# Kernel tuning notes

Measured on AMD Instinct MI355X. Metric: run time of the kernel, lower is better.

Reference implementation:

```python
import jax, jax.numpy as jnp
import numpy as np
import math

B, L, Cs, Cz, Ch, H, Pq, Pv, NB = 1, 768, 384, 128, 16, 12, 4, 8, 30
INF = 100000.0
EPS = 1e-8
HC = H * Ch
CONCAT = H * (Cz + Ch + Pv * 4)


def setup_inputs() -> dict:
    key = jax.random.key(0)
    ks = jax.random.split(key, 24)
    s = jax.random.normal(ks[0], (B, L, Cs), jnp.float32)
    z = jax.random.normal(ks[1], (B, L, NB, Cz), jnp.float32)
    # random orthonormal frames (QR of gaussian) -> valid rigid rotations
    m = jax.random.normal(ks[2], (B, L, 3, 3), jnp.float32)
    rot, _ = jnp.linalg.qr(m)
    trans = jax.random.normal(ks[3], (B, L, 3), jnp.float32) * 10.0
    mask = jnp.ones((B, L), jnp.float32)
    # unique neighbor indices per residue (scatter with duplicate targets is ill-defined)
    E_idx = jnp.argsort(jax.random.uniform(ks[4], (B, L, L)), axis=-1)[..., :NB].astype(jnp.int64)
    sc = 0.02
    W_q = jax.random.normal(ks[5], (Cs, HC), jnp.float32) * sc
    b_q = jnp.zeros((HC,), jnp.float32)
    W_kv = jax.random.normal(ks[6], (Cs, 2 * HC), jnp.float32) * sc
    b_kv = jnp.zeros((2 * HC,), jnp.float32)
    W_qp = jax.random.normal(ks[7], (Cs, H * Pq * 3), jnp.float32) * sc
    b_qp = jnp.zeros((H * Pq * 3,), jnp.float32)
    W_kvp = jax.random.normal(ks[8], (Cs, H * (Pq + Pv) * 3), jnp.float32) * sc
    b_kvp = jnp.zeros((H * (Pq + Pv) * 3,), jnp.float32)
    W_b = jax.random.normal(ks[9], (Cz, H), jnp.float32) * sc
    b_b = jnp.zeros((H,), jnp.float32)
    head_weights = jax.random.normal(ks[10], (H,), jnp.float32) * 0.5 + 0.5
    W_out = jax.random.normal(ks[11], (CONCAT, Cs), jnp.float32) * sc
    b_out = jnp.zeros((Cs,), jnp.float32)
    return dict(s=s, z=z, rot=rot, trans=trans, mask=mask, E_idx=E_idx,
                W_q=W_q, b_q=b_q, W_kv=W_kv, b_kv=b_kv, W_qp=W_qp, b_qp=b_qp,
                W_kvp=W_kvp, b_kvp=b_kvp, W_b=W_b, b_b=b_b,
                head_weights=head_weights, W_out=W_out, b_out=b_out)


def _ipa(s, z, rot, trans, mask, E_idx, W_q, b_q, W_kv, b_kv, W_qp, b_qp,
         W_kvp, b_kvp, W_b, b_b, head_weights, W_out, b_out):
    # scatter neighbor pair features into dense [B, L, L, Cz] (module's z_padding.scatter)
    b_ix = jnp.arange(B)[:, None, None]
    i_ix = jnp.arange(L)[None, :, None]
    z_dense = jnp.zeros((B, L, L, Cz), z.dtype).at[b_ix, i_ix, E_idx].set(z)

    q = (s @ W_q + b_q).reshape(B, L, H, Ch)
    kv = (s @ W_kv + b_kv).reshape(B, L, H, 2 * Ch)
    k, v = kv[..., :Ch], kv[..., Ch:]

    def to_points(flat, P):
        # split into 3 coordinate chunks, stack on last dim -> [B, L, H*P, 3]
        p = jnp.stack(jnp.split(flat, 3, axis=-1), axis=-1)
        # rigid apply: R @ p + t
        p = jnp.einsum('blij,blpj->blpi', rot, p) + trans[:, :, None, :]
        return p.reshape(B, L, H, P, 3)

    q_pts = to_points(s @ W_qp + b_qp, Pq)              # [B,L,H,Pq,3]
    kv_pts = to_points(s @ W_kvp + b_kvp, Pq + Pv)
    k_pts, v_pts = kv_pts[..., :Pq, :], kv_pts[..., Pq:, :]

    bias = z_dense @ W_b + b_b                          # [B,L,L,H]
    a = jnp.einsum('bihc,bjhc->bhij', q, k) * math.sqrt(1.0 / (3 * Ch))
    a = a + math.sqrt(1.0 / 3) * bias.transpose(0, 3, 1, 2)

    # squared point distances [B,L,L,H,Pq]
    diff = q_pts[:, :, None] - k_pts[:, None]           # [B,L,L,H,Pq,3]
    pt_att = jnp.sum(diff * diff, axis=-1)
    hw = jax.nn.softplus(head_weights) * math.sqrt(1.0 / (3 * (Pq * 9.0 / 2)))
    pt_att = jnp.sum(pt_att * hw[None, None, None, :, None], axis=-1) * (-0.5)  # [B,L,L,H]

    sq_mask = INF * (mask[:, :, None] * mask[:, None, :] - 1.0)
    a = a + pt_att.transpose(0, 3, 1, 2) + sq_mask[:, None]
    a = jax.nn.softmax(a, axis=-1)                      # [B,H,L,L]

    o = jnp.einsum('bhij,bjhc->bihc', a, v).reshape(B, L, HC)
    o_pt = jnp.einsum('bhij,bjhpc->bihpc', a, v_pts)    # [B,L,H,Pv,3]
    # rigid invert_apply: R^T (x - t)
    o_pt = jnp.einsum('blji,blhpj->blhpi', rot, o_pt - trans[:, :, None, None, :])
    o_pt_norm = jnp.sqrt(jnp.sum(o_pt ** 2, axis=-1) + EPS).reshape(B, L, H * Pv)
    o_pt = o_pt.reshape(B, L, H * Pv, 3)
    o_pair = jnp.einsum('bhij,bijc->bihc', a, z_dense).reshape(B, L, H * Cz)

    cat = jnp.concatenate(
        [o, o_pt[..., 0], o_pt[..., 1], o_pt[..., 2], o_pt_norm, o_pair], axis=-1)
    return cat @ W_out + b_out


def reference(s, z, rot, trans, mask, E_idx, W_q, b_q, W_kv, b_kv, W_qp, b_qp,
              W_kvp, b_kvp, W_b, b_b, head_weights, W_out, b_out):
    return _ipa(s, z, rot, trans, mask, E_idx, W_q, b_q, W_kv, b_kv, W_qp, b_qp,
                W_kvp, b_kvp, W_b, b_b, head_weights, W_out, b_out)
```

## Files before the change

### kernel.cpp

```cpp
#include <hip/hip_runtime.h>
#include <hip/hip_bf16.h>
#include <math.h>

#define L_    768
#define Cs_   384
#define Cz_   128
#define H_    12
#define NB_   30
#define CONCAT_ 2112
#define PROJN 1152

#define SCALE_QK  0.14433756729740643f
#define SQRT3INV  0.5773502691896258f
#define WC_       0.13608276348795434f
#define INF_      100000.0f

typedef short bf16x8 __attribute__((ext_vector_type(8)));
typedef float f32x4 __attribute__((ext_vector_type(4)));

__device__ __forceinline__ short f2b(float f) {
  __hip_bfloat16 b = __float2bfloat16(f);
  return *reinterpret_cast<short*>(&b);
}
__device__ __forceinline__ float b2f(short s) {
  __hip_bfloat16 b;
  *reinterpret_cast<short*>(&b) = s;
  return __bfloat162float(b);
}

__global__ void pack_kernel(const float* __restrict__ Wq, const float* __restrict__ bq,
                            const float* __restrict__ Wkv, const float* __restrict__ bkv,
                            const float* __restrict__ Wqp, const float* __restrict__ bqp,
                            const float* __restrict__ Wkvp, const float* __restrict__ bkvp,
                            short* __restrict__ WallT, float* __restrict__ ball) {
  int e = blockIdx.x * 256 + threadIdx.x;
  if (e < Cs_ * PROJN) {
    int col = e / 384, kk = e % 384;
    float v;
    if (col < 192)      v = Wq[kk*192 + col];
    else if (col < 576) v = Wkv[kk*384 + (col-192)];
    else if (col < 720) v = Wqp[kk*144 + (col-576)];
    else                v = Wkvp[kk*432 + (col-720)];
    WallT[e] = f2b(v);
  } else if (e < Cs_ * PROJN + PROJN) {
    int col = e - Cs_ * PROJN;
    float v;
    if (col < 192)      v = bq[col];
    else if (col < 576) v = bkv[col-192];
    else if (col < 720) v = bqp[col-576];
    else                v = bkvp[col-720];
    ball[col] = v;
  }
}

__global__ void cvt_s(const float* __restrict__ s, short* __restrict__ sb) {
  int e = blockIdx.x * 256 + threadIdx.x;
  if (e < L_ * Cs_) sb[e] = f2b(s[e]);
}

__global__ __launch_bounds__(64) void proj_mfma(const short* __restrict__ A,
                                                const short* __restrict__ Bt,
                                                const float* __restrict__ bias,
                                                float* __restrict__ C) {
  const int l = threadIdx.x, r = l & 15, kg = l >> 4;
  const int m0 = blockIdx.x * 16, n0 = blockIdx.y * 16;
  const short* ap = A  + (size_t)(m0 + r) * 384 + kg * 8;
  const short* bp = Bt + (size_t)(n0 + r) * 384 + kg * 8;
  f32x4 acc = {0.f, 0.f, 0.f, 0.f};
  #pragma unroll
  for (int k = 0; k < 12; ++k) {
    bf16x8 af = *(const bf16x8*)(ap + k * 32);
    bf16x8 bf = *(const bf16x8*)(bp + k * 32);
    acc = __builtin_amdgcn_mfma_f32_16x16x32_bf16(af, bf, acc, 0, 0, 0);
  }
  const float bv = bias[n0 + r];
  #pragma unroll
  for (int j = 0; j < 4; ++j)
    C[(size_t)(m0 + kg * 4 + j) * PROJN + n0 + r] = acc[j] + bv;
}

__global__ __launch_bounds__(256) void prep_kernel(const float* __restrict__ proj,
                                                   const float* __restrict__ rot,
                                                   const float* __restrict__ trans,
                                                   const float* __restrict__ maskp,
                                                   const float* __restrict__ head_w,
                                                   short* __restrict__ Amat,
                                                   short* __restrict__ Bmat,
                                                   short* __restrict__ VmatT,
                                                   float* __restrict__ colbias) {
  const int h = blockIdx.x / 3;
  const int i = (blockIdx.x % 3) * 256 + threadIdx.x;
  const float* p = proj + (size_t)i * PROJN;
  const float* R = rot + i * 9;
  const float* T = trans + i * 3;
  const float c2 = log1pf(expf(head_w[h])) * WC_;
  short* arow = Amat + ((size_t)h * L_ + i) * 64;
  short* brow = Bmat + ((size_t)h * L_ + i) * 64;
  #pragma unroll
  for (int c = 0; c < 16; ++c) {
    arow[c] = f2b(p[h * 16 + c] * SCALE_QK);
    brow[c] = f2b(p[192 + h * 32 + c]);
    VmatT[((size_t)h * 64 + c) * L_ + i] = f2b(p[192 + h * 32 + 16 + c]);
  }
  #pragma unroll
  for (int pt = 0; pt < 4; ++pt) {
    int idx = h * 4 + pt;
    float lx = p[576 + idx], ly = p[576 + 48 + idx], lz = p[576 + 96 + idx];
    float g[3];
    g[0] = R[0]*lx + R[1]*ly + R[2]*lz + T[0];
    g[1] = R[3]*lx + R[4]*ly + R[5]*lz + T[1];
    g[2] = R[6]*lx + R[7]*ly + R[8]*lz + T[2];
    #pragma unroll
    for (int d = 0; d < 3; ++d) {
      float x = c2 * g[d];
      short xh = f2b(x);
      short xl = f2b(x - b2f(xh));
      arow[16 + pt*3 + d] = xh; arow[28 + pt*3 + d] = xh;
      arow[40 + pt*3 + d] = xl; arow[52 + pt*3 + d] = xl;
    }
  }
  float s2 = 0.f;
  #pragma unroll
  for (int pt = 0; pt < 4; ++pt) {
    int idx = h * 12 + pt;
    float lx = p[720 + idx], ly = p[720 + 144 + idx], lz = p[720 + 288 + idx];
    float g[3];
    g[0] = R[0]*lx + R[1]*ly + R[2]*lz + T[0];
    g[1] = R[3]*lx + R[4]*ly + R[5]*lz + T[1];
    g[2] = R[6]*lx + R[7]*ly + R[8]*lz + T[2];
    #pragma unroll
    for (int d = 0; d < 3; ++d) {
      s2 += g[d] * g[d];
      short kh = f2b(g[d]);
      short kl = f2b(g[d] - b2f(kh));
      brow[16 + pt*3 + d] = kh; brow[28 + pt*3 + d] = kl;
      brow[40 + pt*3 + d] = kh; brow[52 + pt*3 + d] = kl;
    }
  }
  colbias[h * L_ + i] = -0.5f * c2 * s2 + INF_ * (maskp[i] - 1.0f);
  #pragma unroll
  for (int pt = 4; pt < 12; ++pt) {
    int idx = h * 12 + pt;
    float lx = p[720 + idx], ly = p[720 + 144 + idx], lz = p[720 + 288 + idx];
    float g[3];
    g[0] = R[0]*lx + R[1]*ly + R[2]*lz + T[0];
    g[1] = R[3]*lx + R[4]*ly + R[5]*lz + T[1];
    g[2] = R[6]*lx + R[7]*ly + R[8]*lz + T[2];
    #pragma unroll
    for (int d = 0; d < 3; ++d) {
      int pc = (pt - 4) * 3 + d;
      short vh = f2b(g[d]);
      short vl = f2b(g[d] - b2f(vh));
      VmatT[((size_t)h * 64 + 16 + pc) * L_ + i] = vh;
      VmatT[((size_t)h * 64 + 40 + pc) * L_ + i] = vl;
    }
  }
}

__global__ __launch_bounds__(256) void bias_edge_kernel(const float* __restrict__ z,
                                                        const float* __restrict__ Wb,
                                                        float* __restrict__ bias_e) {
  int i = blockIdx.x;
  __shared__ float zs[NB_ * 129];
  __shared__ float wbs[Cz_ * H_];
  int t = threadIdx.x;
  for (int e = t; e < NB_ * Cz_; e += 256) { int k = e >> 7, c = e & 127; zs[k * 129 + c] = z[(size_t)i * NB_ * Cz_ + e]; }
  for (int e = t; e < Cz_ * H_; e += 256) wbs[e] = Wb[e];
  __syncthreads();
  for (int o = t; o < NB_ * H_; o += 256) {
    int k = o / H_, hh = o % H_;
    float a0 = 0.f, a1 = 0.f, a2 = 0.f, a3 = 0.f;
    #pragma unroll
    for (int c = 0; c < 128; c += 4) {
      a0 += zs[k*129 + c    ] * wbs[(c    ) * H_ + hh];
      a1 += zs[k*129 + c + 1] * wbs[(c + 1) * H_ + hh];
      a2 += zs[k*129 + c + 2] * wbs[(c + 2) * H_ + hh];
      a3 += zs[k*129 + c + 3] * wbs[(c + 3) * H_ + hh];
    }
    bias_e[(size_t)i * NB_ * H_ + o] = SQRT3INV * ((a0 + a1) + (a2 + a3));
  }
}

#define SLS 772
__global__ __launch_bounds__(256) void attn_mfma(
    const short* __restrict__ Amat,
    const short* __restrict__ Bmat,
    const short* __restrict__ VmatT,
    const float* __restrict__ colbias,
    const float* __restrict__ bias_e,
    const int*   __restrict__ E_idx,
    const float* __restrict__ rot,
    const float* __restrict__ trans,
    const float* __restrict__ z,
    short* __restrict__ catb)
{
  const int h = blockIdx.y;
  const int i0 = blockIdx.x * 16;
  const int t = threadIdx.x;
  const int lane = t & 63, wave = t >> 6;
  const int fr = lane & 15, kg = lane >> 4;

  __shared__ __align__(16) float Sl[16][SLS];
  __shared__ float ptb[16][48];
  __shared__ float ews[16][NB_];
  __shared__ int   eidx[16][NB_];
  __shared__ float denom[16];

  const short* Ab = Amat + ((size_t)h * L_ + i0 + fr) * 64 + kg * 8;
  bf16x8 a0 = *(const bf16x8*)(Ab);
  bf16x8 a1 = *(const bf16x8*)(Ab + 32);

  for (int e = t; e < 16 * NB_; e += 256)
    eidx[e / NB_][e % NB_] = E_idx[(i0 + e / NB_) * NB_ + e % NB_];

  #pragma unroll 3
  for (int tt = 0; tt < 12; ++tt) {
    const int j0 = wave * 192 + tt * 16;
    const short* Bb = Bmat + ((size_t)h * L_ + j0 + fr) * 64 + kg * 8;
    f32x4 acc = {0.f, 0.f, 0.f, 0.f};
    acc = __builtin_amdgcn_mfma_f32_16x16x32_bf16(a0, *(const bf16x8*)(Bb), acc, 0, 0, 0);
    acc = __builtin_amdgcn_mfma_f32_16x16x32_bf16(a1, *(const bf16x8*)(Bb + 32), acc, 0, 0, 0);
    const float cb = colbias[h * L_ + j0 + fr];
    #pragma unroll
    for (int j = 0; j < 4; ++j)
      Sl[kg * 4 + j][j0 + fr] = acc[j] + cb;
  }
  __syncthreads();

  for (int e = t; e < 16 * NB_; e += 256) {
    int r = e / NB_, k = e % NB_;
    Sl[r][eidx[r][k]] += bias_e[(size_t)((i0 + r) * NB_ + k) * H_ + h];
  }
  __syncthreads();

  {
    const int r = t >> 4, sub = t & 15;
    float mx = -1e30f;
    #pragma unroll
    for (int n = 0; n < 48; ++n) mx = fmaxf(mx, Sl[r][sub + n * 16]);
    #pragma unroll
    for (int d = 8; d; d >>= 1) mx = fmaxf(mx, __shfl_xor(mx, d, 16));
    float sum = 0.f;
    #pragma unroll
    for (int n = 0; n < 48; ++n) {
      float p = __expf(Sl[r][sub + n * 16] - mx);
      Sl[r][sub + n * 16] = p;
      sum += p;
    }
    #pragma unroll
    for (int d = 8; d; d >>= 1) sum += __shfl_xor(sum, d, 16);
    if (sub == 0) denom[r] = sum;
  }
  __syncthreads();

  for (int e = t; e < 16 * NB_; e += 256) {
    int r = e / NB_, k = e % NB_;
    ews[r][k] = Sl[r][eidx[r][k]];
  }

  f32x4 oacc = {0.f, 0.f, 0.f, 0.f};
  const short* Vb = VmatT + ((size_t)h * 64 + wave * 16 + fr) * L_ + kg * 8;
  #pragma unroll 4
  for (int ks = 0; ks < 24; ++ks) {
    const float* sp = &Sl[fr][ks * 32 + kg * 8];
    float4 u = *(const float4*)sp;
    float4 v = *(const float4*)(sp + 4);
    bf16x8 pa;
    pa[0] = f2b(u.x); pa[1] = f2b(u.y); pa[2] = f2b(u.z); pa[3] = f2b(u.w);
    pa[4] = f2b(v.x); pa[5] = f2b(v.y); pa[6] = f2b(v.z); pa[7] = f2b(v.w);
    bf16x8 vb = *(const bf16x8*)(Vb + ks * 32);
    oacc = __builtin_amdgcn_mfma_f32_16x16x32_bf16(pa, vb, oacc, 0, 0, 0);
  }
  if (wave == 0) {
    #pragma unroll
    for (int j = 0; j < 4; ++j) {
      int r = kg * 4 + j;
      catb[(size_t)(i0 + r) * CONCAT_ + h * 16 + fr] = f2b(oacc[j] / denom[r]);
    }
  } else {
    int ch = wave * 16 + fr;
    int dest = (ch < 40) ? (ch - 16) : (24 + ch - 40);
    #pragma unroll
    for (int j = 0; j < 4; ++j)
      ptb[kg * 4 + j][dest] = oacc[j];
  }
  __syncthreads();

  if (t < 128) {
    int r = t >> 3, pt = t & 7;
    int ii = i0 + r;
    float di = 1.0f / denom[r];
    const float* T = trans + ii * 3;
    float gx = (ptb[r][pt * 3 + 0] + ptb[r][24 + pt * 3 + 0]) * di - T[0];
    float gy = (ptb[r][pt * 3 + 1] + ptb[r][24 + pt * 3 + 1]) * di - T[1];
    float gz = (ptb[r][pt * 3 + 2] + ptb[r][24 + pt * 3 + 2]) * di - T[2];
    const float* R = rot + ii * 9;
    float lx = R[0] * gx + R[3] * gy + R[6] * gz;
    float ly = R[1] * gx + R[4] * gy + R[7] * gz;
    float lz = R[2] * gx + R[5] * gy + R[8] * gz;
    float nrm = sqrtf(lx * lx + ly * ly + lz * lz + 1e-8f);
    short* crow = catb + (size_t)ii * CONCAT_;
    crow[192 + h * 8 + pt] = f2b(lx);
    crow[288 + h * 8 + pt] = f2b(ly);
    crow[384 + h * 8 + pt] = f2b(lz);
    crow[480 + h * 8 + pt] = f2b(nrm);
  }

  {
    const int r = t >> 4, sub = t & 15;
    const int ii = i0 + r;
    const float di = 1.0f / denom[r];
    float accs[8];
    #pragma unroll
    for (int n = 0; n < 8; ++n) accs[n] = 0.f;
    #pragma unroll 5
    for (int k = 0; k < NB_; ++k) {
      float w = ews[r][k];
      const float* zp = z + ((size_t)ii * NB_ + k) * Cz_ + sub;
      #pragma unroll
      for (int n = 0; n < 8; ++n) accs[n] += w * zp[n * 16];
    }
    short* crow = catb + (size_t)ii * CONCAT_ + 576 + h * Cz_;
    #pragma unroll
    for (int n = 0; n < 8; ++n) crow[sub + n * 16] = f2b(accs[n] * di);
  }
}

__global__ __launch_bounds__(256) void cvt_wout(const float* __restrict__ W, short* __restrict__ Wt) {
  __shared__ float tile[32][33];
  const int k0 = blockIdx.x * 32, n0 = blockIdx.y * 32;
  const int tn = threadIdx.x & 31, tk = threadIdx.x >> 5;
  #pragma unroll
  for (int kk = tk; kk < 32; kk += 8)
    tile[kk][tn] = W[(size_t)(k0 + kk) * Cs_ + n0 + tn];
  __syncthreads();
  #pragma unroll
  for (int rr = tk; rr < 32; rr += 8)
    Wt[(size_t)(n0 + rr) * CONCAT_ + k0 + tn] = f2b(tile[tn][rr]);
}

__global__ __launch_bounds__(64) void gemm_out_mfma(const short* __restrict__ A,
                                                    const short* __restrict__ Bt,
                                                    const float* __restrict__ bias,
                                                    float* __restrict__ C) {
  const int l = threadIdx.x;
  const int r = l & 15, kg = l >> 4;
  const int m0 = blockIdx.x * 16, n0 = blockIdx.y * 16;
  const short* ap = A  + (size_t)(m0 + r) * CONCAT_ + kg * 8;
  const short* bp = Bt + (size_t)(n0 + r) * CONCAT_ + kg * 8;
  f32x4 acc = {0.f, 0.f, 0.f, 0.f};
  #pragma unroll 6
  for (int k = 0; k < 66; ++k) {
    bf16x8 af = *(const bf16x8*)(ap + k * 32);
    bf16x8 bf = *(const bf16x8*)(bp + k * 32);
    acc = __builtin_amdgcn_mfma_f32_16x16x32_bf16(af, bf, acc, 0, 0, 0);
  }
  const float bv = bias[n0 + r];
  #pragma unroll
  for (int j = 0; j < 4; ++j)
    C[(size_t)(m0 + kg * 4 + j) * Cs_ + n0 + r] = acc[j] + bv;
}

extern "C" void kernel_launch(void* const* d_in, const int* in_sizes, int n_in,
                              void* d_out, int out_size, void* d_ws, size_t ws_size,
                              hipStream_t stream) {
  const float* s      = (const float*)d_in[0];
  const float* z      = (const float*)d_in[1];
  const float* rot    = (const float*)d_in[2];
  const float* trans  = (const float*)d_in[3];
  const float* mask   = (const float*)d_in[4];
  const int*   E      = (const int*)  d_in[5];
  const float* W_q    = (const float*)d_in[6];
  const float* b_q    = (const float*)d_in[7];
  const float* W_kv   = (const float*)d_in[8];
  const float* b_kv   = (const float*)d_in[9];
  const float* W_qp   = (const float*)d_in[10];
  const float* b_qp   = (const float*)d_in[11];
  const float* W_kvp  = (const float*)d_in[12];
  const float* b_kvp  = (const float*)d_in[13];
  const float* W_b    = (const float*)d_in[14];
  const float* b_b    = (const float*)d_in[15];  (void)b_b;
  const float* head_w = (const float*)d_in[16];
  const float* W_out  = (const float*)d_in[17];
  const float* b_out  = (const float*)d_in[18];

  float* ws = (float*)d_ws;
  short* WallT   = (short*)(ws + 0);
  float* ball    = ws + 221184;
  short* sb      = (short*)(ws + 222336);
  float* proj    = ws + 369792;
  short* catb    = (short*)(ws + 0);
  short* WoutT   = (short*)(ws + 811008);
  short* Amat    = (short*)(ws + 1254528);
  short* Bmat    = (short*)(ws + 1549440);
  short* VmatT   = (short*)(ws + 1844352);
  float* colbias = ws + 2139264;
  float* bias_e  = ws + 2148480;

  pack_kernel<<<(Cs_ * PROJN + PROJN + 255) / 256, 256, 0, stream>>>(
      W_q, b_q, W_kv, b_kv, W_qp, b_qp, W_kvp, b_kvp, WallT, ball);

  cvt_s<<<(L_ * Cs_ + 255) / 256, 256, 0, stream>>>(s, sb);

  proj_mfma<<<dim3(L_ / 16, PROJN / 16), 64, 0, stream>>>(sb, WallT, ball, proj);

  prep_kernel<<<36, 256, 0, stream>>>(proj, rot, trans, mask, head_w, Amat, Bmat, VmatT, colbias);

  cvt_wout<<<dim3(CONCAT_ / 32, Cs_ / 32), 256, 0, stream>>>(W_out, WoutT);

  bias_edge_kernel<<<L_, 256, 0, stream>>>(z, W_b, bias_e);

  attn_mfma<<<dim3(L_ / 16, H_), 256, 0, stream>>>(
      Amat, Bmat, VmatT, colbias, bias_e, E, rot, trans, z, catb);

  gemm_out_mfma<<<dim3(L_ / 16, Cs_ / 16), 64, 0, stream>>>(catb, WoutT, b_out, (float*)d_out);
}
```

Measured before the change: 192.6 us.

## Split-K output GEMM, MFMA edge bias, pre-packed bf16 P, fused s conversion

The output GEMM now splits its 66 k-steps across four waves per block and reduces the partials in shared memory, so each block has more waves to hide latency. The edge-bias projection becomes a bf16 MFMA over z rows instead of a scalar shared-memory loop. The attention kernel converts the softmax probabilities to packed bf16 in place once, so the PV loop no longer converts them on every k-step. The s conversion is folded into the weight-pack kernel to remove one launch. The edge bias is now computed in bf16 rather than fp32, which lowers its precision.

```diff
diff --git a/kernel.cpp b/kernel.cpp
--- a/kernel.cpp
+++ b/kernel.cpp
@@ -32,7 +32,9 @@
                             const float* __restrict__ Wkv, const float* __restrict__ bkv,
                             const float* __restrict__ Wqp, const float* __restrict__ bqp,
                             const float* __restrict__ Wkvp, const float* __restrict__ bkvp,
-                            short* __restrict__ WallT, float* __restrict__ ball) {
+                            const float* __restrict__ s,
+                            short* __restrict__ WallT, float* __restrict__ ball,
+                            short* __restrict__ sb) {
   int e = blockIdx.x * 256 + threadIdx.x;
   if (e < Cs_ * PROJN) {
     int col = e / 384, kk = e % 384;
@@ -50,12 +52,10 @@
     else if (col < 720) v = bqp[col-576];
     else                v = bkvp[col-720];
     ball[col] = v;
-  }
-}
-
-__global__ void cvt_s(const float* __restrict__ s, short* __restrict__ sb) {
-  int e = blockIdx.x * 256 + threadIdx.x;
-  if (e < L_ * Cs_) sb[e] = f2b(s[e]);
+  } else if (e < Cs_ * PROJN + PROJN + L_ * Cs_) {
+    int x = e - (Cs_ * PROJN + PROJN);
+    sb[x] = f2b(s[x]);
+  }
 }
 
 __global__ __launch_bounds__(64) void proj_mfma(const short* __restrict__ A,
@@ -157,27 +157,31 @@
   }
 }
 
-__global__ __launch_bounds__(256) void bias_edge_kernel(const float* __restrict__ z,
-                                                        const float* __restrict__ Wb,
-                                                        float* __restrict__ bias_e) {
-  int i = blockIdx.x;
-  __shared__ float zs[NB_ * 129];
-  __shared__ float wbs[Cz_ * H_];
-  int t = threadIdx.x;
-  for (int e = t; e < NB_ * Cz_; e += 256) { int k = e >> 7, c = e & 127; zs[k * 129 + c] = z[(size_t)i * NB_ * Cz_ + e]; }
-  for (int e = t; e < Cz_ * H_; e += 256) wbs[e] = Wb[e];
-  __syncthreads();
-  for (int o = t; o < NB_ * H_; o += 256) {
-    int k = o / H_, hh = o % H_;
-    float a0 = 0.f, a1 = 0.f, a2 = 0.f, a3 = 0.f;
-    #pragma unroll
-    for (int c = 0; c < 128; c += 4) {
-      a0 += zs[k*129 + c    ] * wbs[(c    ) * H_ + hh];
-      a1 += zs[k*129 + c + 1] * wbs[(c + 1) * H_ + hh];
-      a2 += zs[k*129 + c + 2] * wbs[(c + 2) * H_ + hh];
-      a3 += zs[k*129 + c + 3] * wbs[(c + 3) * H_ + hh];
-    }
-    bias_e[(size_t)i * NB_ * H_ + o] = SQRT3INV * ((a0 + a1) + (a2 + a3));
+__global__ __launch_bounds__(64) void bias_mfma(const float* __restrict__ z,
+                                                const float* __restrict__ Wb,
+                                                float* __restrict__ bias_e) {
+  const int l = threadIdx.x, r = l & 15, kg = l >> 4;
+  const int m0 = blockIdx.x * 16;
+  f32x4 acc = {0.f, 0.f, 0.f, 0.f};
+  const float* zr = z + (size_t)(m0 + r) * Cz_ + kg * 8;
+  #pragma unroll
+  for (int kc = 0; kc < 4; ++kc) {
+    float4 a0 = *(const float4*)(zr + kc * 32);
+    float4 a1 = *(const float4*)(zr + kc * 32 + 4);
+    bf16x8 af, bf;
+    af[0]=f2b(a0.x); af[1]=f2b(a0.y); af[2]=f2b(a0.z); af[3]=f2b(a0.w);
+    af[4]=f2b(a1.x); af[5]=f2b(a1.y); af[6]=f2b(a1.z); af[7]=f2b(a1.w);
+    #pragma unroll
+    for (int j = 0; j < 8; ++j) {
+      int k = kc * 32 + kg * 8 + j;
+      bf[j] = (r < H_) ? f2b(Wb[k * H_ + r]) : (short)0;
+    }
+    acc = __builtin_amdgcn_mfma_f32_16x16x32_bf16(af, bf, acc, 0, 0, 0);
+  }
+  if (r < H_) {
+    #pragma unroll
+    for (int j = 0; j < 4; ++j)
+      bias_e[(size_t)(m0 + kg * 4 + j) * H_ + r] = SQRT3INV * acc[j];
   }
 }
 
@@ -257,17 +261,32 @@
     int r = e / NB_, k = e % NB_;
     ews[r][k] = Sl[r][eidx[r][k]];
   }
+  {
+    const int cr = t & 15;
+    const int cc = (t >> 4) * 48;
+    float v[48];
+    #pragma unroll
+    for (int n = 0; n < 12; ++n) {
+      float4 u = *(const float4*)&Sl[cr][cc + n * 4];
+      v[n*4+0] = u.x; v[n*4+1] = u.y; v[n*4+2] = u.z; v[n*4+3] = u.w;
+    }
+    __syncthreads();
+    unsigned* dst = (unsigned*)&Sl[cr][0];
+    #pragma unroll
+    for (int n = 0; n < 24; ++n) {
+      unsigned lo = (unsigned short)f2b(v[2*n]);
+      unsigned hi = (unsigned short)f2b(v[2*n+1]);
+      dst[cc/2 + n] = lo | (hi << 16);
+    }
+  }
+  __syncthreads();
 
   f32x4 oacc = {0.f, 0.f, 0.f, 0.f};
   const short* Vb = VmatT + ((size_t)h * 64 + wave * 16 + fr) * L_ + kg * 8;
+  const short* PbRow = (const short*)&Sl[fr][0];
   #pragma unroll 4
   for (int ks = 0; ks < 24; ++ks) {
-    const float* sp = &Sl[fr][ks * 32 + kg * 8];
-    float4 u = *(const float4*)sp;
-    float4 v = *(const float4*)(sp + 4);
-    bf16x8 pa;
-    pa[0] = f2b(u.x); pa[1] = f2b(u.y); pa[2] = f2b(u.z); pa[3] = f2b(u.w);
-    pa[4] = f2b(v.x); pa[5] = f2b(v.y); pa[6] = f2b(v.z); pa[7] = f2b(v.w);
+    bf16x8 pa = *(const bf16x8*)(PbRow + ks * 32 + kg * 8);
     bf16x8 vb = *(const bf16x8*)(Vb + ks * 32);
     oacc = __builtin_amdgcn_mfma_f32_16x16x32_bf16(pa, vb, oacc, 0, 0, 0);
   }
@@ -339,26 +358,33 @@
     Wt[(size_t)(n0 + rr) * CONCAT_ + k0 + tn] = f2b(tile[tn][rr]);
 }
 
-__global__ __launch_bounds__(64) void gemm_out_mfma(const short* __restrict__ A,
-                                                    const short* __restrict__ Bt,
-                                                    const float* __restrict__ bias,
-                                                    float* __restrict__ C) {
-  const int l = threadIdx.x;
+__global__ __launch_bounds__(256) void gemm_out_mfma(const short* __restrict__ A,
+                                                     const short* __restrict__ Bt,
+                                                     const float* __restrict__ bias,
+                                                     float* __restrict__ C) {
+  const int t = threadIdx.x;
+  const int w = t >> 6, l = t & 63;
   const int r = l & 15, kg = l >> 4;
   const int m0 = blockIdx.x * 16, n0 = blockIdx.y * 16;
-  const short* ap = A  + (size_t)(m0 + r) * CONCAT_ + kg * 8;
-  const short* bp = Bt + (size_t)(n0 + r) * CONCAT_ + kg * 8;
+  __shared__ float part[4][16][17];
+  const int kcnt = (w < 2) ? 17 : 16;
+  const int koff = (w < 2) ? w * 17 : 34 + (w - 2) * 16;
+  const short* ap = A  + (size_t)(m0 + r) * CONCAT_ + koff * 32 + kg * 8;
+  const short* bp = Bt + (size_t)(n0 + r) * CONCAT_ + koff * 32 + kg * 8;
   f32x4 acc = {0.f, 0.f, 0.f, 0.f};
-  #pragma unroll 6
-  for (int k = 0; k < 66; ++k) {
+  #pragma unroll 4
+  for (int k = 0; k < kcnt; ++k) {
     bf16x8 af = *(const bf16x8*)(ap + k * 32);
     bf16x8 bf = *(const bf16x8*)(bp + k * 32);
     acc = __builtin_amdgcn_mfma_f32_16x16x32_bf16(af, bf, acc, 0, 0, 0);
   }
-  const float bv = bias[n0 + r];
-  #pragma unroll
-  for (int j = 0; j < 4; ++j)
-    C[(size_t)(m0 + kg * 4 + j) * Cs_ + n0 + r] = acc[j] + bv;
+  #pragma unroll
+  for (int j = 0; j < 4; ++j) part[w][kg * 4 + j][r] = acc[j];
+  __syncthreads();
+  const int row = t >> 4, col = t & 15;
+  float sum = part[0][row][col] + part[1][row][col]
+            + part[2][row][col] + part[3][row][col] + bias[n0 + col];
+  C[(size_t)(m0 + row) * Cs_ + n0 + col] = sum;
 }
 
 extern "C" void kernel_launch(void* const* d_in, const int* in_sizes, int n_in,
@@ -397,10 +423,8 @@
   float* colbias = ws + 2139264;
   float* bias_e  = ws + 2148480;
 
-  pack_kernel<<<(Cs_ * PROJN + PROJN + 255) / 256, 256, 0, stream>>>(
-      W_q, b_q, W_kv, b_kv, W_qp, b_qp, W_kvp, b_kvp, WallT, ball);
-
-  cvt_s<<<(L_ * Cs_ + 255) / 256, 256, 0, stream>>>(s, sb);
+  pack_kernel<<<(Cs_ * PROJN + PROJN + L_ * Cs_ + 255) / 256, 256, 0, stream>>>(
+      W_q, b_q, W_kv, b_kv, W_qp, b_qp, W_kvp, b_kvp, s, WallT, ball, sb);
 
   proj_mfma<<<dim3(L_ / 16, PROJN / 16), 64, 0, stream>>>(sb, WallT, ball, proj);
 
@@ -408,10 +432,10 @@
 
   cvt_wout<<<dim3(CONCAT_ / 32, Cs_ / 32), 256, 0, stream>>>(W_out, WoutT);
 
-  bias_edge_kernel<<<L_, 256, 0, stream>>>(z, W_b, bias_e);
+  bias_mfma<<<(L_ * NB_) / 16, 64, 0, stream>>>(z, W_b, bias_e);
 
   attn_mfma<<<dim3(L_ / 16, H_), 256, 0, stream>>>(
       Amat, Bmat, VmatT, colbias, bias_e, E, rot, trans, z, catb);
 
-  gemm_out_mfma<<<dim3(L_ / 16, Cs_ / 16), 64, 0, stream>>>(catb, WoutT, b_out, (float*)d_out);
-}
+  gemm_out_mfma<<<dim3(L_ / 16, Cs_ / 16), 256, 0, stream>>>(catb, WoutT, b_out, (float*)d_out);
+}
```

After: 187.2 us. 2.8% less time.
